# Optimization experiments

Hardware: AMD Instinct MI355X
Metric: run time of the kernel (lower is better)

The kernel has to match this reference:

```python
import jax, jax.numpy as jnp
import numpy as np

# ---- module geometry ----
BULK = 64          # bulk (J2) integration points, 3 comps each
COH = 32           # cohesive integration points, 2 comps each
LS = BULK * 3 + COH * 2  # = 256, material layer width

# ---- J2 plasticity material constants (plane-stress, linear isotropic hardening) ----
E_MOD = 200.0
NU = 0.3
SY0 = 2.0
HARD = 10.0
G_MOD = E_MOD / (2.0 * (1.0 + NU))
_c = E_MOD / (1.0 - NU * NU)
C_EL = np.array([[_c, _c * NU, 0.0], [_c * NU, _c, 0.0], [0.0, 0.0, _c * (1.0 - NU) / 2.0]], dtype=np.float32)
C_INV = np.linalg.inv(C_EL).astype(np.float32)

# ---- Turon cohesive-zone constants (bilinear damage law) ----
K_PEN = 50.0       # penalty stiffness
DELTA0 = 0.1       # damage-onset effective jump
DELTAF = 1.0       # full-failure effective jump


def j2_update(eps, epsp, epbar):
    # eps, epsp: [B,P,3]; epbar: [B,P]. Radial-return with linear hardening.
    sig_tr = jnp.einsum('bpi,ji->bpj', eps - epsp, jnp.asarray(C_EL))
    s1, s2, s12 = sig_tr[..., 0], sig_tr[..., 1], sig_tr[..., 2]
    seq = jnp.sqrt(jnp.maximum(s1 * s1 - s1 * s2 + s2 * s2 + 3.0 * s12 * s12, 1e-12))
    f = seq - (SY0 + HARD * epbar)
    plastic = f > 0.0
    dep = jnp.where(plastic, f / (3.0 * G_MOD + HARD), 0.0)
    r = (SY0 + HARD * (epbar + dep)) / seq
    sig = jnp.where(plastic[..., None], r[..., None] * sig_tr, sig_tr)
    epsp_new = jnp.where(plastic[..., None], eps - jnp.einsum('bpj,ij->bpi', sig, jnp.asarray(C_INV)), epsp)
    return sig, epsp_new, epbar + dep


def coh_update(jump, hist):
    # jump: [B,P,2] (normal, shear); hist: [B,P] max effective jump (damage history).
    dn, ds = jump[..., 0], jump[..., 1]
    lam = jnp.sqrt(jnp.maximum(jnp.maximum(dn, 0.0) ** 2 + ds * ds, 1e-12))
    hist_new = jnp.maximum(hist, lam)
    dmg = jnp.clip(DELTAF * (hist_new - DELTA0) / (jnp.maximum(hist_new, 1e-12) * (DELTAF - DELTA0)), 0.0, 1.0)
    tn = K_PEN * dn * jnp.where(dn > 0.0, 1.0 - dmg, 1.0)  # compression is undamaged
    ts = (1.0 - dmg) * K_PEN * ds
    return jnp.stack([tn, ts], axis=-1), hist_new


def setup_inputs() -> dict:
    key = jax.random.key(0)
    k1, k2, k3 = jax.random.split(key, 3)
    x = jax.random.normal(k1, (256, 1024, 16), dtype=jnp.float32)
    W1 = jax.random.normal(k2, (LS, 16), dtype=jnp.float32) * 0.1
    W2 = jax.random.normal(k3, (16, LS), dtype=jnp.float32) * 0.1
    return {"x": x, "W1": W1, "W2": W2}


def reference(x, W1, W2):
    B, T, F = x.shape
    # fc1 applied to every (batch, time) slice (original loops; here one GEMM)
    h = jnp.einsum('btf,lf->btl', x, W1)  # [B,T,LS]
    h_t = jnp.transpose(h, (1, 0, 2))     # [T,B,LS] for the time scan

    epsp0 = jnp.zeros((B, BULK, 3), dtype=x.dtype)
    epbar0 = jnp.zeros((B, BULK), dtype=x.dtype)
    hist0 = jnp.zeros((B, COH), dtype=x.dtype)

    def step(carry, ht):
        epsp, epbar, hist = carry
        eps = ht[:, : BULK * 3].reshape(B, BULK, 3)
        jmp = ht[:, BULK * 3:].reshape(B, COH, 2)
        sig, epsp, epbar = j2_update(eps, epsp, epbar)   # update + commit per step
        trac, hist = coh_update(jmp, hist)
        y = jnp.concatenate([sig.reshape(B, -1), trac.reshape(B, -1)], axis=-1)
        return (epsp, epbar, hist), y

    _, ys = jax.lax.scan(step, (epsp0, epbar0, hist0), h_t)  # [T,B,LS]
    ys = jnp.transpose(ys, (1, 0, 2))  # [B,T,LS]
    # softLayer fc2: linear with softplus-constrained (non-negative) weights
    out = jnp.einsum('btl,ol->bto', ys, jax.nn.softplus(W2))
    return out
```

## Files before the change

### kernel.cpp

```cpp
#include <hip/hip_runtime.h>
#include <cmath>
#include <cstdint>

#define BATCH  256
#define TT     1024
#define FIN    16
#define TC     32
#define NCHUNK (TT / TC)
#define SROW   324
#define YSS    328
#define HB     16

typedef __attribute__((ext_vector_type(8))) short short8;
typedef __attribute__((ext_vector_type(4))) float floatx4;

__device__ __forceinline__ unsigned short f2bf_rne(float f) {
    union { float f; unsigned int i; } v; v.f = f;
    unsigned int b = v.i;
    return (unsigned short)((b + 0x7FFFu + ((b >> 16) & 1u)) >> 16);
}
__device__ __forceinline__ float u2f(unsigned int u) {
    union { unsigned int i; float f; } v; v.i = u; return v.f;
}

#define SBAR()  __builtin_amdgcn_sched_barrier(0)
#define ACQ()   asm volatile("" ::: "memory")
#define REL()   asm volatile("s_waitcnt lgkmcnt(0)" ::: "memory")

#define MC00   219.78021978021977f
#define MC01   65.93406593406593f
#define MC22   76.92307692307692f
#define MSY0   2.0f
#define AK     0.958466453674121406f
#define BK     0.041533546325878594f


__global__ __launch_bounds__(512, 2)
void fused_mat_kernel(const float* __restrict__ x,
                      const float* __restrict__ w1,
                      const float* __restrict__ w2,
                      float* __restrict__ out)
{
    __shared__ __attribute__((aligned(16))) float          s_h[2][TC][SROW];
    __shared__ __attribute__((aligned(16))) unsigned short s_y[2][TC][YSS];
    __shared__ int flg[16];

    volatile int* F = (volatile int*)flg;

    const int tid  = threadIdx.x;
    const int b    = blockIdx.x;
    const int lane = tid & 63;
    const int wv   = tid >> 6;
    const int m    = lane & 15;
    const int q    = lane >> 4;

    const size_t xrow = (size_t)b * TT;

    const bool isG   = (wv == 2) | (wv == 3) | (wv == 6) | (wv == 7);
    const int  hw    = (wv == 2) ? 0 : (wv == 3) ? 1 : (wv == 6) ? 2 : 3;
    const int  nbase = hw * 5;

    short8 wfrag[5];
    short8 vf[10];
    uint4  rxc[2][2], rxp[2][2];

    if (tid == 0) {
        flg[4] = -1; flg[5] = -1; flg[6] = -1; flg[7] = -1; flg[8] = -1; flg[9] = -1;
    }

    auto emit = [&](const short8* axv, const short8* adxv, float* dst) {
        #pragma unroll
        for (int mt = 0; mt < 2; ++mt) {
            float* drow = dst + (mt * 16 + m) * SROW + q * 4 + nbase * 16;
            #pragma unroll
            for (int j = 0; j < 5; ++j) {
                const int n = nbase + j;
                floatx4 acc = {0.f, 0.f, 0.f, 0.f};
                acc = __builtin_amdgcn_mfma_f32_16x16x32_bf16(
                        wfrag[j], (n < 16) ? adxv[mt] : axv[mt], acc, 0, 0, 0);
                *(floatx4*)(drow + j * 16) = acc;
            }
        }
    };

    if (isG) {
        #pragma unroll
        for (int j = 0; j < 5; ++j) {
            const int n = nbase + j;
            #pragma unroll
            for (int jj = 0; jj < 8; ++jj) {
                float v = 0.f;
                if (q < 2) {
                    const int f = q * 8 + jj;
                    if (n < 16) {
                        const int lp = n * 16 + m, c = lp >> 2, cm = lp & 3;
                        if (cm < 3) {
                            const float wa  = w1[(3 * c + 0) * FIN + f];
                            const float wb  = w1[(3 * c + 1) * FIN + f];
                            const float wcc = w1[(3 * c + 2) * FIN + f];
                            v = (cm == 0) ? fmaf(MC01, wb, MC00 * wa)
                              : (cm == 1) ? fmaf(MC00, wb, MC01 * wa)
                                          : MC22 * wcc;
                        }
                    } else {
                        v = w1[(192 + (n - 16) * 16 + m) * FIN + f];
                    }
                }
                wfrag[j][jj] = (short)f2bf_rne(v);
            }
        }
        short8 ax0[2], adx0[2];
        #pragma unroll
        for (int mt = 0; mt < 2; ++mt) {
            #pragma unroll
            for (int j = 0; j < 8; ++j) {
                float xc = 0.f, xp = 0.f;
                if (q < 2) {
                    const int rowB = mt * 16 + m;
                    xc = x[(xrow + rowB) * FIN + q * 8 + j];
                    if (rowB > 0) xp = x[(xrow + rowB - 1) * FIN + q * 8 + j];
                }
                ax0[mt][j]  = (short)f2bf_rne(xc);
                adx0[mt][j] = (short)f2bf_rne(xc - xp);
            }
        }
        if (q < 2) {
            #pragma unroll
            for (int mt = 0; mt < 2; ++mt) {
                const int rowB = TC + mt * 16 + m;
                const float* xc = x + (xrow + rowB) * FIN + q * 8;
                const float* xp = x + (xrow + rowB - 1) * FIN + q * 8;
                rxc[mt][0] = *(const uint4*)xc;  rxc[mt][1] = *(const uint4*)(xc + 4);
                rxp[mt][0] = *(const uint4*)xp;  rxp[mt][1] = *(const uint4*)(xp + 4);
            }
        }
        emit(ax0, adx0, &s_h[0][0][0]);
        if (lane == 0) flg[hw] = 0;
    } else if (wv == 4 || wv == 5) {
        #pragma unroll
        for (int ks = 0; ks < 10; ++ks) {
            #pragma unroll
            for (int j = 0; j < 8; ++j) {
                const int p = ks * 32 + q * 8 + j;
                unsigned short v = 0;
                if (p < 256) {
                    const int comp = p & 3;
                    if (comp < 3) {
                        const int l = 3 * (p >> 2) + comp;
                        float xv = w2[m * 256 + l];
                        float sp = fmaxf(xv, 0.0f) + log1pf(expf(-fabsf(xv)));
                        v = f2bf_rne(sp);
                    }
                } else {
                    const int l = p - 64;
                    float xv = w2[m * 256 + l];
                    float sp = fmaxf(xv, 0.0f) + log1pf(expf(-fabsf(xv)));
                    v = f2bf_rne(sp);
                }
                vf[ks][j] = (short)v;
            }
        }
    }

    float tt0 = 0.f, tt1 = 0.f, tt2 = 0.f, rr = 1.0f, syv = MSY0, pre = AK * MSY0;
    float hist = 0.f;

    __syncthreads();

    if (wv == 0) {
        for (int i = 0; i < NCHUNK; ++i) {
            while (F[0] < i) {} while (F[1] < i) {} while (F[2] < i) {} while (F[3] < i) {}
            const int yf = i - 2;
            while (F[8] < yf) {} while (F[9] < yf) {}
            ACQ();
            const float* hb = &s_h[i & 1][0][0] + 4 * lane;
            unsigned short* yb = &s_y[i & 1][0][0] + 4 * lane;
            floatx4 dvvA[HB], dvvB[HB];
            uint2   yreg[TC];
            #pragma unroll
            for (int t = 0; t < HB; ++t) dvvA[t] = *(const floatx4*)(hb + t * SROW);
            SBAR();
            #pragma unroll
            for (int t = 0; t < HB; ++t) dvvB[t] = *(const floatx4*)(hb + (HB + t) * SROW);
            SBAR();
            #pragma unroll
            for (int t = 0; t < TC; ++t) {
                const floatx4 dv = (t < HB) ? dvvA[t] : dvvB[t - HB];
                tt0 = fmaf(rr, tt0, dv.x);
                tt1 = fmaf(rr, tt1, dv.y);
                tt2 = fmaf(rr, tt2, dv.z);
                const float s01 = tt0 - tt1;
                const float u   = tt2 * tt2;
                const float w3  = fmaf(u, 3.0f, 1e-12f);
                const float bb  = fmaf(tt1, tt1, w3);
                const float qq  = fmaf(tt0, s01, bb);
                const float rs  = __builtin_amdgcn_rsqf(qq);
                const float seq = qq * rs;
                rr  = fminf(fmaf(pre, rs, BK), 1.0f);
                syv = fmaxf(syv, fmaf(BK, seq, pre));
                pre = AK * syv;
                const float sg0 = rr * tt0, sg1 = rr * tt1, sg2 = rr * tt2;
                unsigned int r0, r1;
                asm("v_cvt_pk_bf16_f32 %0, %1, %2" : "=v"(r0) : "v"(sg0), "v"(sg1));
                asm("v_cvt_pk_bf16_f32 %0, %1, %2" : "=v"(r1) : "v"(sg2), "v"(sg2));
                yreg[t].x = r0; yreg[t].y = r1;
            }
            SBAR();
            #pragma unroll
            for (int t = 0; t < TC; ++t)
                *(uint2*)(yb + t * YSS) = yreg[t];
            REL();
            if (lane == 0) { F[4] = i; F[6] = i; }
        }
    } else if (wv == 1) {
        for (int i = 0; i < NCHUNK; ++i) {
            while (F[3] < i) {}
            const int yf = i - 2;
            while (F[8] < yf) {} while (F[9] < yf) {}
            ACQ();
            if (lane < 32) {
                const float* hc = &s_h[i & 1][0][0] + 256 + 2 * lane;
                unsigned short* yc = &s_y[i & 1][0][0] + 256 + 2 * lane;
                float2 jvv[TC];
                unsigned int yr[TC];
                #pragma unroll
                for (int t = 0; t < TC; ++t) jvv[t] = *(const float2*)(hc + t * SROW);
                SBAR();
                #pragma unroll
                for (int t = 0; t < TC; ++t) {
                    const float dn = jvv[t].x, ds = jvv[t].y;
                    const float dnp = fmaxf(dn, 0.0f);
                    const float lam = __builtin_amdgcn_sqrtf(fmaxf(fmaf(dnp, dnp, ds * ds), 1e-12f));
                    hist = fmaxf(hist, lam);
                    float dmg = (hist - 0.1f) * __builtin_amdgcn_rcpf(hist * 0.9f);
                    dmg = fminf(fmaxf(dmg, 0.0f), 1.0f);
                    const float om = 1.0f - dmg;
                    const float tn = 50.0f * dn * (dn > 0.0f ? om : 1.0f);
                    const float ts = om * 50.0f * ds;
                    unsigned int r;
                    asm("v_cvt_pk_bf16_f32 %0, %1, %2" : "=v"(r) : "v"(tn), "v"(ts));
                    yr[t] = r;
                }
                SBAR();
                #pragma unroll
                for (int t = 0; t < TC; ++t)
                    *(unsigned int*)(yc + t * YSS) = yr[t];
            }
            REL();
            if (lane == 0) { F[5] = i; F[7] = i; }
        }
    } else if (isG) {
        for (int k = 1; k < NCHUNK; ++k) {
            short8 ax[2], adx[2];
            #pragma unroll
            for (int mt = 0; mt < 2; ++mt) {
                const unsigned int wc[8] = {rxc[mt][0].x, rxc[mt][0].y, rxc[mt][0].z, rxc[mt][0].w,
                                            rxc[mt][1].x, rxc[mt][1].y, rxc[mt][1].z, rxc[mt][1].w};
                const unsigned int wp[8] = {rxp[mt][0].x, rxp[mt][0].y, rxp[mt][0].z, rxp[mt][0].w,
                                            rxp[mt][1].x, rxp[mt][1].y, rxp[mt][1].z, rxp[mt][1].w};
                union { unsigned int u[4]; short8 s; } Ua, Ud;
                #pragma unroll
                for (int p = 0; p < 4; ++p) {
                    const float c0 = u2f(wc[2 * p]),          c1 = u2f(wc[2 * p + 1]);
                    const float d0 = c0 - u2f(wp[2 * p]),     d1 = c1 - u2f(wp[2 * p + 1]);
                    unsigned int va, vd;
                    asm("v_cvt_pk_bf16_f32 %0, %1, %2" : "=v"(va) : "v"(c0), "v"(c1));
                    asm("v_cvt_pk_bf16_f32 %0, %1, %2" : "=v"(vd) : "v"(d0), "v"(d1));
                    Ua.u[p] = (q < 2) ? va : 0u;
                    Ud.u[p] = (q < 2) ? vd : 0u;
                }
                ax[mt]  = Ua.s;
                adx[mt] = Ud.s;
            }
            if (k + 1 < NCHUNK && q < 2) {
                #pragma unroll
                for (int mt = 0; mt < 2; ++mt) {
                    const int rowB = (k + 1) * TC + mt * 16 + m;
                    const float* xc = x + (xrow + rowB) * FIN + q * 8;
                    const float* xp = x + (xrow + rowB - 1) * FIN + q * 8;
                    rxc[mt][0] = *(const uint4*)xc;  rxc[mt][1] = *(const uint4*)(xc + 4);
                    rxp[mt][0] = *(const uint4*)xp;  rxp[mt][1] = *(const uint4*)(xp + 4);
                }
            }
            const int hf = k - 2;
            while (F[4] < hf) __builtin_amdgcn_s_sleep(1);
            if (hw == 3) { while (F[5] < hf) __builtin_amdgcn_s_sleep(1); }
            ACQ();
            emit(ax, adx, &s_h[k & 1][0][0]);
            REL();
            if (lane == 0) F[hw] = k;
        }
    } else {
        const int mt = wv - 4;
        for (int j = 0; j < NCHUNK; ++j) {
            while (F[6] < j) __builtin_amdgcn_s_sleep(1);
            while (F[7] < j) __builtin_amdgcn_s_sleep(1);
            ACQ();
            const int tb = j * TC;
            const unsigned short* yb = &s_y[j & 1][0][0];
            floatx4 a0 = {0.f, 0.f, 0.f, 0.f};
            floatx4 a1 = {0.f, 0.f, 0.f, 0.f};
            #pragma unroll
            for (int ks = 0; ks < 5; ++ks) {
                const short8* yp = (const short8*)(yb + (mt * 16 + m) * YSS + ks * 32 + q * 8);
                a0 = __builtin_amdgcn_mfma_f32_16x16x32_bf16(*yp, vf[ks], a0, 0, 0, 0);
            }
            #pragma unroll
            for (int ks = 5; ks < 10; ++ks) {
                const short8* yp = (const short8*)(yb + (mt * 16 + m) * YSS + ks * 32 + q * 8);
                a1 = __builtin_amdgcn_mfma_f32_16x16x32_bf16(*yp, vf[ks], a1, 0, 0, 0);
            }
            #pragma unroll
            for (int r = 0; r < 4; ++r)
                out[(xrow + tb + mt * 16 + q * 4 + r) * FIN + m] = a0[r] + a1[r];
            REL();
            if (lane == 0) F[8 + mt] = j;
        }
    }
}

extern "C" void kernel_launch(void* const* d_in, const int* in_sizes, int n_in,
                              void* d_out, int out_size, void* d_ws, size_t ws_size,
                              hipStream_t stream) {
    const float* x  = (const float*)d_in[0];
    const float* w1 = (const float*)d_in[1];
    const float* w2 = (const float*)d_in[2];
    float* out = (float*)d_out;
    fused_mat_kernel<<<BATCH, 512, 0, stream>>>(x, w1, w2, out);
}
```

Before: 150.9 us.

## Release input buffer flags early and batch flag polling with sleep

The J2 and cohesive waves now signal that the h buffer is consumed right after loading it into registers, instead of after writing outputs. This lets the GEMM producer waves refill it while the recurrence computes. The wait on the y-buffer consumers moves to just before the y stores. Flag polls are merged into combined multi-flag loops with s_sleep backoff, which cuts LDS polling traffic. The extra sleep may add wake-up latency on the critical serial recurrence path.

```diff
diff --git a/kernel.cpp b/kernel.cpp
--- a/kernel.cpp
+++ b/kernel.cpp
@@ -26,6 +26,17 @@
 #define SBAR()  __builtin_amdgcn_sched_barrier(0)
 #define ACQ()   asm volatile("" ::: "memory")
 #define REL()   asm volatile("s_waitcnt lgkmcnt(0)" ::: "memory")
+
+#define POLL4GE(i0, val) \
+    for (;;) { int f0_=F[i0], f1_=F[(i0)+1], f2_=F[(i0)+2], f3_=F[(i0)+3]; \
+        if (f0_>=(val) && f1_>=(val) && f2_>=(val) && f3_>=(val)) break; \
+        __builtin_amdgcn_s_sleep(1); }
+#define POLL2GE(i0, val) \
+    for (;;) { int f0_=F[i0], f1_=F[(i0)+1]; \
+        if (f0_>=(val) && f1_>=(val)) break; \
+        __builtin_amdgcn_s_sleep(1); }
+#define POLL1GE(i0, val) \
+    for (;;) { int f0_=F[i0]; if (f0_>=(val)) break; __builtin_amdgcn_s_sleep(1); }
 
 #define MC00   219.78021978021977f
 #define MC01   65.93406593406593f
@@ -169,9 +180,7 @@
 
     if (wv == 0) {
         for (int i = 0; i < NCHUNK; ++i) {
-            while (F[0] < i) {} while (F[1] < i) {} while (F[2] < i) {} while (F[3] < i) {}
-            const int yf = i - 2;
-            while (F[8] < yf) {} while (F[9] < yf) {}
+            POLL4GE(0, i);
             ACQ();
             const float* hb = &s_h[i & 1][0][0] + 4 * lane;
             unsigned short* yb = &s_y[i & 1][0][0] + 4 * lane;
@@ -182,6 +191,8 @@
             SBAR();
             #pragma unroll
             for (int t = 0; t < HB; ++t) dvvB[t] = *(const floatx4*)(hb + (HB + t) * SROW);
+            REL();
+            if (lane == 0) F[4] = i;
             SBAR();
             #pragma unroll
             for (int t = 0; t < TC; ++t) {
@@ -206,17 +217,17 @@
                 yreg[t].x = r0; yreg[t].y = r1;
             }
             SBAR();
+            POLL2GE(8, i - 2);
+            ACQ();
             #pragma unroll
             for (int t = 0; t < TC; ++t)
                 *(uint2*)(yb + t * YSS) = yreg[t];
             REL();
-            if (lane == 0) { F[4] = i; F[6] = i; }
+            if (lane == 0) F[6] = i;
         }
     } else if (wv == 1) {
         for (int i = 0; i < NCHUNK; ++i) {
-            while (F[3] < i) {}
-            const int yf = i - 2;
-            while (F[8] < yf) {} while (F[9] < yf) {}
+            POLL1GE(3, i);
             ACQ();
             if (lane < 32) {
                 const float* hc = &s_h[i & 1][0][0] + 256 + 2 * lane;
@@ -225,6 +236,8 @@
                 unsigned int yr[TC];
                 #pragma unroll
                 for (int t = 0; t < TC; ++t) jvv[t] = *(const float2*)(hc + t * SROW);
+                REL();
+                if (lane == 0) F[5] = i;
                 SBAR();
                 #pragma unroll
                 for (int t = 0; t < TC; ++t) {
@@ -242,12 +255,16 @@
                     yr[t] = r;
                 }
                 SBAR();
+                POLL2GE(8, i - 2);
+                ACQ();
                 #pragma unroll
                 for (int t = 0; t < TC; ++t)
                     *(unsigned int*)(yc + t * YSS) = yr[t];
-            }
-            REL();
-            if (lane == 0) { F[5] = i; F[7] = i; }
+            } else {
+                if (lane == 32) { POLL1GE(3, i); }
+            }
+            REL();
+            if (lane == 0) F[7] = i;
         }
     } else if (isG) {
         for (int k = 1; k < NCHUNK; ++k) {
@@ -283,8 +300,8 @@
                 }
             }
             const int hf = k - 2;
-            while (F[4] < hf) __builtin_amdgcn_s_sleep(1);
-            if (hw == 3) { while (F[5] < hf) __builtin_amdgcn_s_sleep(1); }
+            if (hw == 3) { POLL2GE(4, hf); }
+            else        { POLL1GE(4, hf); }
             ACQ();
             emit(ax, adx, &s_h[k & 1][0][0]);
             REL();
@@ -293,8 +310,7 @@
     } else {
         const int mt = wv - 4;
         for (int j = 0; j < NCHUNK; ++j) {
-            while (F[6] < j) __builtin_amdgcn_s_sleep(1);
-            while (F[7] < j) __builtin_amdgcn_s_sleep(1);
+            POLL2GE(6, j);
             ACQ();
             const int tb = j * TC;
             const unsigned short* yb = &s_y[j & 1][0][0];
```

Measured after the change: 146.4 us. -3.0%, faster.
